# Kernel tuning notes

Measured on AMD Instinct MI355X. Metric: run time of the kernel, lower is better.

Reference implementation:

```python
import jax, jax.numpy as jnp
import numpy as np

B, S, D_IN, D_OUT, H = 4, 2048, 1024, 1024, 16
HD = D_OUT // H


def setup_inputs() -> dict:
    key = jax.random.key(0)
    ks = jax.random.split(key, 6)
    s_in = 1.0 / np.sqrt(D_IN)
    s_out = 1.0 / np.sqrt(D_OUT)
    return {
        "x": jax.random.normal(ks[0], (B, S, D_IN), dtype=jnp.float32),
        "W_q": jax.random.uniform(ks[1], (D_OUT, D_IN), jnp.float32, -s_in, s_in),
        "W_k": jax.random.uniform(ks[2], (D_OUT, D_IN), jnp.float32, -s_in, s_in),
        "W_v": jax.random.uniform(ks[3], (D_OUT, D_IN), jnp.float32, -s_in, s_in),
        "W_o": jax.random.uniform(ks[4], (D_OUT, D_OUT), jnp.float32, -s_out, s_out),
        "b_o": jax.random.uniform(ks[5], (D_OUT,), jnp.float32, -s_out, s_out),
    }


def reference(x, W_q, W_k, W_v, W_o, b_o):
    b, s, _ = x.shape
    # torch Linear: y = x @ W.T  (no qkv bias)
    q = (x @ W_q.T).reshape(b, s, H, HD).transpose(0, 2, 1, 3)  # [b,h,s,hd]
    k = (x @ W_k.T).reshape(b, s, H, HD).transpose(0, 2, 1, 3)
    v = (x @ W_v.T).reshape(b, s, H, HD).transpose(0, 2, 1, 3)
    scores = jnp.einsum("bhqd,bhkd->bhqk", q, k)  # [b,h,s,s]
    causal = jnp.triu(jnp.ones((s, s), dtype=bool), k=1)
    scores = jnp.where(causal, -jnp.inf, scores)
    attn = jax.nn.softmax(scores / np.sqrt(HD), axis=-1)
    # dropout p=0.0 -> identity
    ctx = jnp.einsum("bhqk,bhkd->bhqd", attn, v)  # [b,h,s,hd]
    ctx = ctx.transpose(0, 2, 1, 3).reshape(b, s, D_OUT)
    return ctx @ W_o.T + b_o
```

## Files before the change

### kernel.cpp

```cpp
#include <hip/hip_runtime.h>
#include <cstdint>
#include <cstddef>

#define S_LEN  2048
#define NHEAD  16
#define HDIM   64
#define KD     1024
#define BSROWS 8192

typedef __attribute__((ext_vector_type(4))) float          floatx4;
typedef __attribute__((ext_vector_type(8))) __bf16         bf16x8;
typedef __attribute__((ext_vector_type(8))) unsigned short ushort8v;
typedef __attribute__((ext_vector_type(4))) unsigned short ushort4v;
typedef __attribute__((ext_vector_type(4))) float          float4v;

__device__ __forceinline__ unsigned short f2bf(float f) {
  unsigned int u = __float_as_uint(f);
  u += 0x7fffu + ((u >> 16) & 1u);
  return (unsigned short)(u >> 16);
}

#if __has_builtin(__builtin_amdgcn_exp2f)
#define EXP2F(x) __builtin_amdgcn_exp2f(x)
#else
#define EXP2F(x) exp2f(x)
#endif

__device__ __forceinline__ unsigned int pack2bf(float a, float b) {
#if __has_builtin(__builtin_amdgcn_perm)
  return __builtin_amdgcn_perm(__float_as_uint(b), __float_as_uint(a), 0x07060302);
#else
  return (__float_as_uint(a) >> 16) | (__float_as_uint(b) & 0xffff0000u);
#endif
}

__device__ __forceinline__ void async_cp16(const void* gsrc, void* ldst) {
  __builtin_amdgcn_global_load_lds(
      (__attribute__((address_space(1))) void*)gsrc,
      (__attribute__((address_space(3))) void*)ldst,
      16, 0, 0);
}

#define XN4 2097152
#define WN4 262144

__global__ __launch_bounds__(256) void cvt_kernel(
    const float* __restrict__ x,  const float* __restrict__ wq,
    const float* __restrict__ wk, const float* __restrict__ wv,
    const float* __restrict__ wo,
    unsigned short* __restrict__ xb, unsigned short* __restrict__ wqkvb,
    unsigned short* __restrict__ wob)
{
  const int i = blockIdx.x * 256 + threadIdx.x;
  const float* src; unsigned short* dst; int off;
  if (i < XN4) { src = x; dst = xb; off = i; }
  else {
    const int j = i - XN4;
    if (j < WN4)          { src = wq; dst = wqkvb;           off = j; }
    else if (j < 2*WN4)   { src = wk; dst = wqkvb + 4*WN4;   off = j - WN4; }
    else if (j < 3*WN4)   { src = wv; dst = wqkvb + 8*WN4;   off = j - 2*WN4; }
    else                  { src = wo; dst = wob;             off = j - 3*WN4; }
  }
  const float4v v = ((const float4v*)src)[off];
  ushort4v o;
  o.x = f2bf(v.x); o.y = f2bf(v.y); o.z = f2bf(v.z); o.w = f2bf(v.w);
  ((ushort4v*)dst)[off] = o;
}

__global__ __launch_bounds__(256) void gemm_qkv(
    const unsigned short* __restrict__ A,
    const unsigned short* __restrict__ Bw,
    unsigned short* __restrict__ Qo,
    unsigned short* __restrict__ Ko,
    unsigned short* __restrict__ Vto)
{
  __shared__ unsigned short smem[17408];
  unsigned short* As = smem;
  unsigned short* Bs = smem + 4096;
  const int tid  = threadIdx.x;
  const int wave = tid >> 6, lane = tid & 63;
  const int quad = lane >> 4, l15 = lane & 15;
  const int wr = wave >> 1, wc = wave & 1;
  const int m0 = blockIdx.x * 128, n0 = blockIdx.y * 128;

  const int srow = lane >> 2;
  const int scol = (lane & 3) * 8;
  const unsigned short* gA = A  + (size_t)(m0 + wave * 32 + srow) * KD + scol;
  const unsigned short* gB = Bw + (size_t)(n0 + wave * 32 + srow) * KD + scol;
  unsigned short* lA = &As[wave * 32 * 32];
  unsigned short* lB = &Bs[wave * 32 * 32];

  const floatx4 fzero = {0.f, 0.f, 0.f, 0.f};
  floatx4 acc[4][4];
#pragma unroll
  for (int i = 0; i < 4; i++)
#pragma unroll
    for (int j = 0; j < 4; j++) acc[i][j] = fzero;

  for (int k0 = 0; k0 < KD; k0 += 32) {
    __syncthreads();
    async_cp16(gA + k0,                 lA);
    async_cp16(gA + k0 + (size_t)16*KD, lA + 16 * 32);
    async_cp16(gB + k0,                 lB);
    async_cp16(gB + k0 + (size_t)16*KD, lB + 16 * 32);
    __syncthreads();

    bf16x8 af[4], bfrag[4];
#pragma unroll
    for (int i = 0; i < 4; i++)
      af[i] = *(const bf16x8*)&As[(wr * 64 + i * 16 + l15) * 32 + quad * 8];
#pragma unroll
    for (int j = 0; j < 4; j++)
      bfrag[j] = *(const bf16x8*)&Bs[(wc * 64 + j * 16 + l15) * 32 + quad * 8];
#pragma unroll
    for (int i = 0; i < 4; i++)
#pragma unroll
      for (int j = 0; j < 4; j++)
        acc[i][j] = __builtin_amdgcn_mfma_f32_16x16x32_bf16(af[i], bfrag[j], acc[i][j], 0, 0, 0);
  }

  const int which = n0 >> 10;
  const int h0 = (n0 & 1023) >> 6;
  const int b = m0 >> 11, sl = m0 & 2047;

  if (which < 2) {
    unsigned short* dst = which ? Ko : Qo;
    const float scale = which ? 1.0f : 0.18033688011112042f;
    __syncthreads();
    const int crow = wr * 64 + quad * 4;
    const int ccol = wc * 64 + l15;
#pragma unroll
    for (int i = 0; i < 4; i++)
#pragma unroll
      for (int j = 0; j < 4; j++)
#pragma unroll
        for (int r = 0; r < 4; r++)
          smem[(crow + i * 16 + r) * 130 + ccol + j * 16] = f2bf(acc[i][j][r] * scale);
    __syncthreads();
#pragma unroll
    for (int t = 0; t < 8; t++) {
      const int c   = t * 256 + tid;
      const int hd8 = (c & 7) * 8;
      const int hh  = (c >> 3) & 1;
      const int s   = c >> 4;
      const ushort8v val = *(const ushort8v*)&smem[s * 130 + hh * 64 + hd8];
      *(ushort8v*)&dst[((size_t)((b * NHEAD + h0 + hh) * S_LEN + sl + s)) * HDIM + hd8] = val;
    }
  } else {
    __syncthreads();
    const int crow = wr * 64 + quad * 4;
    const int ccol = wc * 64 + l15;
#pragma unroll
    for (int i = 0; i < 4; i++)
#pragma unroll
      for (int j = 0; j < 4; j++) {
        ushort4v t4;
#pragma unroll
        for (int r = 0; r < 4; r++) t4[r] = f2bf(acc[i][j][r]);
        *(ushort4v*)&smem[(ccol + j * 16) * 136 + crow + i * 16] = t4;
      }
    __syncthreads();
#pragma unroll
    for (int t = 0; t < 8; t++) {
      const int c  = t * 256 + tid;
      const int nl = c >> 4, sc = (c & 15) * 8;
      const ushort8v val = *(const ushort8v*)&smem[nl * 136 + sc];
      *(ushort8v*)&Vto[((size_t)((b * NHEAD + h0 + (nl >> 6)) * HDIM + (nl & 63))) * S_LEN + sl + sc] = val;
    }
  }
}

__global__ __launch_bounds__(512, 4) void attn_kernel(
    const unsigned short* __restrict__ Qg_,
    const unsigned short* __restrict__ Kg_,
    const unsigned short* __restrict__ Vtg_,
    unsigned short* __restrict__ CTX)
{
  __shared__ unsigned short smem[33792];
  const int tid  = threadIdx.x, wave = tid >> 6, lane = tid & 63;
  const int quad = lane >> 4, l15 = lane & 15;
  unsigned short* Pw = smem + 16384 + wave * 2176;

  const int bh = (int)blockIdx.x;
  const int yy = (int)blockIdx.y;
  const int qt = (yy < 4) ? yy : (11 - yy);
  const int q0 = qt * 256;
  const size_t base = (size_t)bh * (S_LEN * HDIM);
  const unsigned short* Qg  = Qg_  + base;
  const unsigned short* Kg  = Kg_  + base;
  const unsigned short* Vtg = Vtg_ + base;
  const int qw = q0 + wave * 32;

  const int strow = lane >> 3;
  const int stxc  = (lane & 7) ^ strow;
  const unsigned short* kstage = Kg  + (size_t)(wave * 8 + strow) * HDIM  + stxc * 8;
  const unsigned short* vstage = Vtg + (size_t)(wave * 8 + strow) * S_LEN + stxc * 8;
  unsigned short* kd0 = smem + wave * 512;
  unsigned short* vd0 = smem + 4096 + wave * 512;

  async_cp16(kstage, kd0);
  async_cp16(vstage, vd0);

  bf16x8 qf[2][2];
#pragma unroll
  for (int qtile = 0; qtile < 2; qtile++)
#pragma unroll
    for (int ks = 0; ks < 2; ks++)
      qf[qtile][ks] = *(const bf16x8*)&Qg[(size_t)(qw + qtile * 16 + l15) * HDIM + ks * 32 + quad * 8];

  const int sw0 = ((quad)     ^ (l15 & 7)) * 8;
  const int sw1 = ((4 + quad) ^ (l15 & 7)) * 8;

  const floatx4 fzero = {0.f, 0.f, 0.f, 0.f};
  floatx4 O[2][4];
  float l_part[2] = {0.f, 0.f};
#pragma unroll
  for (int qtile = 0; qtile < 2; qtile++)
#pragma unroll
    for (int mt = 0; mt < 4; mt++) O[qtile][mt] = fzero;

  const int ntiles = 4 * (qt + 1);

  for (int j = 0; j < ntiles; j++) {
    asm volatile("s_waitcnt vmcnt(0) lgkmcnt(0)\n\ts_barrier" ::: "memory");
    if (j + 1 < ntiles) {
      const int nb = (j + 1) & 1;
      async_cp16(kstage + (size_t)(j + 1) * 64 * HDIM, kd0 + nb * 8192);
      async_cp16(vstage + (size_t)(j + 1) * 64,        vd0 + nb * 8192);
    }
    const int k0 = j * 64;
    if (k0 > qw + 31) continue;
    const unsigned short* Ksb = smem + (j & 1) * 8192;
    const unsigned short* Vsb = Ksb + 4096;
    const int krel = qw + 31 - k0;

    bf16x8 kf[4][2];
#pragma unroll
    for (int kt = 0; kt < 4; kt++) {
      if (kt * 16 <= krel) {
        const unsigned short* kr = &Ksb[(kt * 16 + l15) * 64];
        kf[kt][0] = *(const bf16x8*)(kr + sw0);
        kf[kt][1] = *(const bf16x8*)(kr + sw1);
      }
    }

#pragma unroll
    for (int qtile = 0; qtile < 2; qtile++) {
      const int kmax = qw + qtile * 16 + 15;
      if (k0 > kmax) continue;
      floatx4 sa[4];
#pragma unroll
      for (int kt = 0; kt < 4; kt++) sa[kt] = fzero;
#pragma unroll
      for (int kt = 0; kt < 4; kt++) {
        if (k0 + kt * 16 <= kmax) {
          sa[kt] = __builtin_amdgcn_mfma_f32_16x16x32_bf16(kf[kt][0], qf[qtile][0], sa[kt], 0, 0, 0);
          sa[kt] = __builtin_amdgcn_mfma_f32_16x16x32_bf16(kf[kt][1], qf[qtile][1], sa[kt], 0, 0, 0);
        }
      }
      const int qrow = qw + qtile * 16 + l15;
#pragma unroll
      for (int kt = 0; kt < 4; kt++) {
        const int kbase = k0 + kt * 16;
        unsigned short* pdst = &Pw[(qtile * 16 + l15) * 68 + kt * 16 + quad * 4];
        if (kbase <= kmax) {
          if (kbase + 15 > qw + qtile * 16) {
#pragma unroll
            for (int r = 0; r < 4; r++)
              if (kbase + quad * 4 + r > qrow) sa[kt][r] = -INFINITY;
          }
          const float p0 = EXP2F(sa[kt][0]), p1 = EXP2F(sa[kt][1]);
          const float p2 = EXP2F(sa[kt][2]), p3 = EXP2F(sa[kt][3]);
          l_part[qtile] += (p0 + p1) + (p2 + p3);
          uint2 pk; pk.x = pack2bf(p0, p1); pk.y = pack2bf(p2, p3);
          *(uint2*)pdst = pk;
        } else if (k0 + (kt >> 1) * 32 <= kmax) {
          uint2 z; z.x = 0u; z.y = 0u;
          *(uint2*)pdst = z;
        }
      }
    }
    asm volatile("s_waitcnt lgkmcnt(0)" ::: "memory");

#pragma unroll
    for (int ks = 0; ks < 2; ks++) {
      if (ks * 32 > krel) break;
      bf16x8 vf[4];
#pragma unroll
      for (int mt = 0; mt < 4; mt++)
        vf[mt] = *(const bf16x8*)(&Vsb[(mt * 16 + l15) * 64] + (ks ? sw1 : sw0));
#pragma unroll
      for (int qtile = 0; qtile < 2; qtile++) {
        if (k0 + ks * 32 > qw + qtile * 16 + 15) continue;
        const unsigned short* ps = &Pw[(qtile * 16 + l15) * 68 + ks * 32 + quad * 8];
        union { ushort4v h[2]; bf16x8 v; } pu;
        pu.h[0] = *(const ushort4v*)ps;
        pu.h[1] = *(const ushort4v*)(ps + 4);
#pragma unroll
        for (int mt = 0; mt < 4; mt++)
          O[qtile][mt] = __builtin_amdgcn_mfma_f32_16x16x32_bf16(vf[mt], pu.v, O[qtile][mt], 0, 0, 0);
      }
    }
  }

#pragma unroll
  for (int d = 16; d < 64; d <<= 1) {
    l_part[0] += __shfl_xor(l_part[0], d, 64);
    l_part[1] += __shfl_xor(l_part[1], d, 64);
  }

#pragma unroll
  for (int qtile = 0; qtile < 2; qtile++) {
    const float inv = 1.0f / l_part[qtile];
#pragma unroll
    for (int mt = 0; mt < 4; mt++)
#pragma unroll
      for (int a = 0; a < 2; a++) {
        const unsigned int pk =
            (unsigned int)f2bf(O[qtile][mt][2 * a] * inv) |
            ((unsigned int)f2bf(O[qtile][mt][2 * a + 1] * inv) << 16);
        *(unsigned int*)&Pw[(qtile * 16 + l15) * 68 + mt * 16 + quad * 4 + 2 * a] = pk;
      }
  }
  asm volatile("s_waitcnt lgkmcnt(0)" ::: "memory");
  const int b = bh >> 4, h = bh & 15;
#pragma unroll
  for (int it = 0; it < 4; it++) {
    const int g = it * 64 + lane;
    const int row = g >> 3, c8 = (g & 7) * 8;
    union { ushort4v h[2]; ushort8v v; } ou;
    ou.h[0] = *(const ushort4v*)&Pw[row * 68 + c8];
    ou.h[1] = *(const ushort4v*)&Pw[row * 68 + c8 + 4];
    const int s = qw + row;
    *(ushort8v*)&CTX[((size_t)(b * S_LEN + s)) * KD + h * HDIM + c8] = ou.v;
  }
}

__global__ __launch_bounds__(256) void gemm_out(
    const unsigned short* __restrict__ A,
    const unsigned short* __restrict__ Bw,
    const float* __restrict__ bias,
    float* __restrict__ out)
{
  __shared__ unsigned short As[128 * 32];
  __shared__ unsigned short Bs[128 * 32];
  const int tid  = threadIdx.x;
  const int wave = tid >> 6, lane = tid & 63;
  const int quad = lane >> 4, l15 = lane & 15;
  const int wr = wave >> 1, wc = wave & 1;
  const int m0 = blockIdx.x * 128, n0 = blockIdx.y * 128;

  const int srow = lane >> 2;
  const int scol = (lane & 3) * 8;
  const unsigned short* gA = A  + (size_t)(m0 + wave * 32 + srow) * KD + scol;
  const unsigned short* gB = Bw + (size_t)(n0 + wave * 32 + srow) * KD + scol;
  unsigned short* lA = &As[wave * 32 * 32];
  unsigned short* lB = &Bs[wave * 32 * 32];

  const floatx4 fzero = {0.f, 0.f, 0.f, 0.f};
  floatx4 acc[4][4];
#pragma unroll
  for (int i = 0; i < 4; i++)
#pragma unroll
    for (int j = 0; j < 4; j++) acc[i][j] = fzero;

  for (int k0 = 0; k0 < KD; k0 += 32) {
    __syncthreads();
    async_cp16(gA + k0,                 lA);
    async_cp16(gA + k0 + (size_t)16*KD, lA + 16 * 32);
    async_cp16(gB + k0,                 lB);
    async_cp16(gB + k0 + (size_t)16*KD, lB + 16 * 32);
    __syncthreads();

    bf16x8 af[4], bfrag[4];
#pragma unroll
    for (int i = 0; i < 4; i++)
      af[i] = *(const bf16x8*)&As[(wr * 64 + i * 16 + l15) * 32 + quad * 8];
#pragma unroll
    for (int j = 0; j < 4; j++)
      bfrag[j] = *(const bf16x8*)&Bs[(wc * 64 + j * 16 + l15) * 32 + quad * 8];
#pragma unroll
    for (int i = 0; i < 4; i++)
#pragma unroll
      for (int j = 0; j < 4; j++)
        acc[i][j] = __builtin_amdgcn_mfma_f32_16x16x32_bf16(af[i], bfrag[j], acc[i][j], 0, 0, 0);
  }

#pragma unroll
  for (int j = 0; j < 4; j++) {
    const int n = n0 + wc * 64 + j * 16 + l15;
    const float bb = bias[n];
#pragma unroll
    for (int i = 0; i < 4; i++) {
#pragma unroll
      for (int r = 0; r < 4; r++) {
        const int m = m0 + wr * 64 + i * 16 + quad * 4 + r;
        out[(size_t)m * KD + n] = acc[i][j][r] + bb;
      }
    }
  }
}

extern "C" void kernel_launch(void* const* d_in, const int* in_sizes, int n_in,
                              void* d_out, int out_size, void* d_ws, size_t ws_size,
                              hipStream_t stream) {
  (void)in_sizes; (void)n_in; (void)out_size;
  const float* x  = (const float*)d_in[0];
  const float* wq = (const float*)d_in[1];
  const float* wk = (const float*)d_in[2];
  const float* wv = (const float*)d_in[3];
  const float* wo = (const float*)d_in[4];
  const float* bo = (const float*)d_in[5];
  float* out = (float*)d_out;

  if (ws_size < (size_t)92274688) return;
  char* ws = (char*)d_ws;
  unsigned short* xb    = (unsigned short*)(ws);
  unsigned short* wqkvb = (unsigned short*)(ws + (size_t)16777216);
  unsigned short* wob   = (unsigned short*)(ws + (size_t)23068672);
  unsigned short* qws   = (unsigned short*)(ws + (size_t)25165824);
  unsigned short* kws   = (unsigned short*)(ws + (size_t)41943040);
  unsigned short* vtws  = (unsigned short*)(ws + (size_t)58720256);
  unsigned short* ctxws = (unsigned short*)(ws + (size_t)75497472);

  cvt_kernel<<<12288, 256, 0, stream>>>(x, wq, wk, wv, wo, xb, wqkvb, wob);
  gemm_qkv<<<dim3(64, 24), 256, 0, stream>>>(xb, wqkvb, qws, kws, vtws);
  attn_kernel<<<dim3(64, 8), 512, 0, stream>>>(qws, kws, vtws, ctxws);
  gemm_out<<<dim3(64, 8), 256, 0, stream>>>(ctxws, wob, bo, out);
}
```

Before: 259.4 us.

## Double-buffer LDS tiles and swizzle columns in QKV and output GEMMs

Both projection GEMMs now prefetch the next K tile into a second LDS buffer while computing on the current one, using one barrier per iteration instead of two. The LDS column index is XOR-swizzled on write and read to reduce bank conflicts when loading MFMA fragments. This doubles shared memory use per block for the GEMMs, which may reduce occupancy.

```diff
diff --git a/kernel.cpp b/kernel.cpp
--- a/kernel.cpp
+++ b/kernel.cpp
@@ -75,8 +75,6 @@
     unsigned short* __restrict__ Vto)
 {
   __shared__ unsigned short smem[17408];
-  unsigned short* As = smem;
-  unsigned short* Bs = smem + 4096;
   const int tid  = threadIdx.x;
   const int wave = tid >> 6, lane = tid & 63;
   const int quad = lane >> 4, l15 = lane & 15;
@@ -84,11 +82,9 @@
   const int m0 = blockIdx.x * 128, n0 = blockIdx.y * 128;
 
   const int srow = lane >> 2;
-  const int scol = (lane & 3) * 8;
+  const int scol = ((lane & 3) ^ ((srow >> 1) & 3)) * 8;
   const unsigned short* gA = A  + (size_t)(m0 + wave * 32 + srow) * KD + scol;
   const unsigned short* gB = Bw + (size_t)(n0 + wave * 32 + srow) * KD + scol;
-  unsigned short* lA = &As[wave * 32 * 32];
-  unsigned short* lB = &Bs[wave * 32 * 32];
 
   const floatx4 fzero = {0.f, 0.f, 0.f, 0.f};
   floatx4 acc[4][4];
@@ -97,21 +93,39 @@
 #pragma unroll
     for (int j = 0; j < 4; j++) acc[i][j] = fzero;
 
-  for (int k0 = 0; k0 < KD; k0 += 32) {
-    __syncthreads();
-    async_cp16(gA + k0,                 lA);
-    async_cp16(gA + k0 + (size_t)16*KD, lA + 16 * 32);
-    async_cp16(gB + k0,                 lB);
-    async_cp16(gB + k0 + (size_t)16*KD, lB + 16 * 32);
-    __syncthreads();
+  {
+    unsigned short* lA = smem + wave * 1024;
+    unsigned short* lB = smem + 4096 + wave * 1024;
+    async_cp16(gA,                    lA);
+    async_cp16(gA + (size_t)16 * KD,  lA + 512);
+    async_cp16(gB,                    lB);
+    async_cp16(gB + (size_t)16 * KD,  lB + 512);
+  }
+  const int lsw = (l15 >> 1) & 3;
+
+#pragma unroll 2
+  for (int it = 0; it < 32; it++) {
+    asm volatile("s_waitcnt vmcnt(0) lgkmcnt(0)\n\ts_barrier" ::: "memory");
+    if (it + 1 < 32) {
+      const int nb = (it + 1) & 1;
+      const int ko = (it + 1) * 32;
+      unsigned short* lA = smem + nb * 8192 + wave * 1024;
+      unsigned short* lB = smem + nb * 8192 + 4096 + wave * 1024;
+      async_cp16(gA + ko,                   lA);
+      async_cp16(gA + ko + (size_t)16 * KD, lA + 512);
+      async_cp16(gB + ko,                   lB);
+      async_cp16(gB + ko + (size_t)16 * KD, lB + 512);
+    }
+    const unsigned short* As = smem + (it & 1) * 8192;
+    const unsigned short* Bs = As + 4096;
 
     bf16x8 af[4], bfrag[4];
 #pragma unroll
     for (int i = 0; i < 4; i++)
-      af[i] = *(const bf16x8*)&As[(wr * 64 + i * 16 + l15) * 32 + quad * 8];
+      af[i] = *(const bf16x8*)&As[(wr * 64 + i * 16 + l15) * 32 + (quad ^ lsw) * 8];
 #pragma unroll
     for (int j = 0; j < 4; j++)
-      bfrag[j] = *(const bf16x8*)&Bs[(wc * 64 + j * 16 + l15) * 32 + quad * 8];
+      bfrag[j] = *(const bf16x8*)&Bs[(wc * 64 + j * 16 + l15) * 32 + (quad ^ lsw) * 8];
 #pragma unroll
     for (int i = 0; i < 4; i++)
 #pragma unroll
@@ -342,8 +356,7 @@
     const float* __restrict__ bias,
     float* __restrict__ out)
 {
-  __shared__ unsigned short As[128 * 32];
-  __shared__ unsigned short Bs[128 * 32];
+  __shared__ unsigned short smem[16384];
   const int tid  = threadIdx.x;
   const int wave = tid >> 6, lane = tid & 63;
   const int quad = lane >> 4, l15 = lane & 15;
@@ -351,11 +364,9 @@
   const int m0 = blockIdx.x * 128, n0 = blockIdx.y * 128;
 
   const int srow = lane >> 2;
-  const int scol = (lane & 3) * 8;
+  const int scol = ((lane & 3) ^ ((srow >> 1) & 3)) * 8;
   const unsigned short* gA = A  + (size_t)(m0 + wave * 32 + srow) * KD + scol;
   const unsigned short* gB = Bw + (size_t)(n0 + wave * 32 + srow) * KD + scol;
-  unsigned short* lA = &As[wave * 32 * 32];
-  unsigned short* lB = &Bs[wave * 32 * 32];
 
   const floatx4 fzero = {0.f, 0.f, 0.f, 0.f};
   floatx4 acc[4][4];
@@ -364,21 +375,39 @@
 #pragma unroll
     for (int j = 0; j < 4; j++) acc[i][j] = fzero;
 
-  for (int k0 = 0; k0 < KD; k0 += 32) {
-    __syncthreads();
-    async_cp16(gA + k0,                 lA);
-    async_cp16(gA + k0 + (size_t)16*KD, lA + 16 * 32);
-    async_cp16(gB + k0,                 lB);
-    async_cp16(gB + k0 + (size_t)16*KD, lB + 16 * 32);
-    __syncthreads();
+  {
+    unsigned short* lA = smem + wave * 1024;
+    unsigned short* lB = smem + 4096 + wave * 1024;
+    async_cp16(gA,                    lA);
+    async_cp16(gA + (size_t)16 * KD,  lA + 512);
+    async_cp16(gB,                    lB);
+    async_cp16(gB + (size_t)16 * KD,  lB + 512);
+  }
+  const int lsw = (l15 >> 1) & 3;
+
+#pragma unroll 2
+  for (int it = 0; it < 32; it++) {
+    asm volatile("s_waitcnt vmcnt(0) lgkmcnt(0)\n\ts_barrier" ::: "memory");
+    if (it + 1 < 32) {
+      const int nb = (it + 1) & 1;
+      const int ko = (it + 1) * 32;
+      unsigned short* lA = smem + nb * 8192 + wave * 1024;
+      unsigned short* lB = smem + nb * 8192 + 4096 + wave * 1024;
+      async_cp16(gA + ko,                   lA);
+      async_cp16(gA + ko + (size_t)16 * KD, lA + 512);
+      async_cp16(gB + ko,                   lB);
+      async_cp16(gB + ko + (size_t)16 * KD, lB + 512);
+    }
+    const unsigned short* As = smem + (it & 1) * 8192;
+    const unsigned short* Bs = As + 4096;
 
     bf16x8 af[4], bfrag[4];
 #pragma unroll
     for (int i = 0; i < 4; i++)
-      af[i] = *(const bf16x8*)&As[(wr * 64 + i * 16 + l15) * 32 + quad * 8];
+      af[i] = *(const bf16x8*)&As[(wr * 64 + i * 16 + l15) * 32 + (quad ^ lsw) * 8];
 #pragma unroll
     for (int j = 0; j < 4; j++)
-      bfrag[j] = *(const bf16x8*)&Bs[(wc * 64 + j * 16 + l15) * 32 + quad * 8];
+      bfrag[j] = *(const bf16x8*)&Bs[(wc * 64 + j * 16 + l15) * 32 + (quad ^ lsw) * 8];
 #pragma unroll
     for (int i = 0; i < 4; i++)
 #pragma unroll
```

Measured after the change: 252.8 us. 1.03x faster.
